# Performance work log

Hardware: AMD Instinct MI355X
Metric: run time of the kernel (lower is better)

Reference implementation:

```python
import jax, jax.numpy as jnp
import numpy as np

B, C_IN, T = 32, 192, 8192
H, N_PH, OUT = 192, 1024, 4
EPS = 1e-5


def setup_inputs() -> dict:
    key = jax.random.key(0)
    ks = jax.random.split(key, 12)
    s = 0.02
    return {
        "x": jax.random.normal(ks[0], (B, C_IN, T), jnp.float32),
        "x_mask": jnp.ones((B, 1, N_PH), jnp.float32),
        "w": jax.random.randint(ks[1], (B, 1, N_PH), 0, 8, jnp.int32),
        "pre_w": jax.random.normal(ks[2], (H, C_IN), jnp.float32) * s,
        "pre_b": jnp.zeros((H,), jnp.float32),
        "conv0_w": jax.random.normal(ks[3], (H, H, 3), jnp.float32) * s,
        "conv0_b": jnp.zeros((H,), jnp.float32),
        "ln0_g": jnp.ones((H,), jnp.float32),
        "ln0_b": jnp.zeros((H,), jnp.float32),
        "conv1_w": jax.random.normal(ks[4], (H, H, 3), jnp.float32) * s,
        "conv1_b": jnp.zeros((H,), jnp.float32),
        "ln1_g": jnp.ones((H,), jnp.float32),
        "ln1_b": jnp.zeros((H,), jnp.float32),
        "lin_w": jax.random.normal(ks[5], (OUT, H), jnp.float32) * s,
        "lin_b": jnp.zeros((OUT,), jnp.float32),
    }


def _segment_mean(x, w2):
    # x: [B, C, T] frames; w2: [B, n_ph] int durations.
    # Faithful to the torch double loop: phoneme j pools frames
    # [cumsum(w)[j-1] : cumsum(w)[j]); w==0 -> zeros.
    ends = jnp.cumsum(w2, axis=1)                      # [B, n_ph]
    t = jnp.arange(x.shape[2], dtype=ends.dtype)       # [T]
    ph_id = jax.vmap(lambda e: jnp.searchsorted(e, t, side="right"))(ends)  # [B, T]
    # segment sums over frames; extra segment n_ph catches out-of-range frames
    sums = jax.vmap(lambda xt, ids: jax.ops.segment_sum(xt, ids, num_segments=N_PH + 1))(
        x.transpose(0, 2, 1), ph_id
    )                                                  # [B, n_ph+1, C]
    sums = sums[:, :N_PH].transpose(0, 2, 1)           # [B, C, n_ph]
    denom = jnp.maximum(w2, 1).astype(x.dtype)[:, None, :]
    return jnp.where(w2[:, None, :] > 0, sums / denom, 0.0)


def _conv3(x, k, b):
    y = jax.lax.conv_general_dilated(x, k, (1,), [(1, 1)],
                                     dimension_numbers=("NCH", "OIH", "NCH"))
    return y + b[None, :, None]


def _ln(x, g, b):
    # channel-dim LayerNorm for [B, C, T] (VITS modules.LayerNorm)
    m = jnp.mean(x, axis=1, keepdims=True)
    v = jnp.mean(jnp.square(x - m), axis=1, keepdims=True)
    return (x - m) * jax.lax.rsqrt(v + EPS) * g[None, :, None] + b[None, :, None]


def reference(x, x_mask, w, pre_w, pre_b, conv0_w, conv0_b, ln0_g, ln0_b,
              conv1_w, conv1_b, ln1_g, ln1_b, lin_w, lin_b):
    w2 = w.reshape(w.shape[0], -1).astype(jnp.int32)
    spec = _segment_mean(x, w2)                                 # [B, C_in, n_ph]
    h = jnp.einsum("bct,hc->bht", spec, pre_w) + pre_b[None, :, None]
    # block 0: conv -> relu -> LN (dropout is identity at eval), mask before each layer
    h = _conv3(h * x_mask, conv0_w, conv0_b)
    h = jax.nn.relu(h * x_mask)
    h = _ln(h * x_mask, ln0_g, ln0_b)
    h = h * x_mask  # dropout(p=0.1) at eval = identity; mask still applied
    # block 1
    h = _conv3(h * x_mask, conv1_w, conv1_b)
    h = jax.nn.relu(h * x_mask)
    h = _ln(h * x_mask, ln1_g, ln1_b)
    h = h * x_mask
    p = jnp.einsum("bht,oh->bot", h, lin_w) + lin_b[None, :, None]
    return p * x_mask
```

## Files before the change

kernel.cpp:

```cpp
#include <hip/hip_runtime.h>
#include <hip/hip_bf16.h>

#define B 32
#define C_IN 192
#define T 8192
#define H 192
#define N_PH 1024
#define OUT 4
#define ROW_MAX 7168
#define PROWS (N_PH + 2)
#define ROWP (2 * H)

typedef __attribute__((ext_vector_type(8))) short short8;
typedef __attribute__((ext_vector_type(4))) float f32x4;
typedef unsigned short ushort_t;

__device__ inline ushort_t f2bf(float f) {
    unsigned u = __builtin_bit_cast(unsigned, f);
    unsigned r = u + 0x7fffu + ((u >> 16) & 1u);
    return (ushort_t)(r >> 16);
}
__device__ inline float bf2f(ushort_t h) {
    unsigned u = ((unsigned)h) << 16;
    return __builtin_bit_cast(float, u);
}
__device__ inline void split_bf(float x, ushort_t& hi, ushort_t& lo) {
    hi = f2bf(x);
    lo = f2bf(x - bf2f(hi));
}

__global__ __launch_bounds__(256) void segmean_kernel(const float* __restrict__ x,
                                                      const int* __restrict__ wdur,
                                                      float* __restrict__ spec) {
    int bc = blockIdx.x;
    int b = bc / C_IN;
    int c = bc % C_IN;
    __shared__ int e_s[N_PH];
    __shared__ int part[256];
    __shared__ float row[ROW_MAX];
    int tid = threadIdx.x;
    int4 w4 = ((const int4*)(wdur + b * N_PH))[tid];
    int c0 = w4.x, c1 = c0 + w4.y, c2 = c1 + w4.z, c3 = c2 + w4.w;
    part[tid] = c3;
    __syncthreads();
    for (int off = 1; off < 256; off <<= 1) {
        int v = (tid >= off) ? part[tid - off] : 0;
        __syncthreads();
        part[tid] += v;
        __syncthreads();
    }
    int pre = tid ? part[tid - 1] : 0;
    e_s[4 * tid + 0] = pre + c0;
    e_s[4 * tid + 1] = pre + c1;
    e_s[4 * tid + 2] = pre + c2;
    e_s[4 * tid + 3] = pre + c3;
    __syncthreads();
    int emax = e_s[N_PH - 1];
    const float4* xr4 = (const float4*)(x + ((size_t)b * C_IN + c) * T);
    float4* row4 = (float4*)row;
    int nv = (emax + 3) >> 2;
    for (int t = tid; t < nv; t += 256) row4[t] = xr4[t];
    __syncthreads();
    float* sp = spec + ((size_t)b * C_IN + c) * N_PH;
    for (int j = tid; j < N_PH; j += 256) {
        int s0 = j ? e_s[j - 1] : 0;
        int e0 = e_s[j];
        float sum = 0.f;
        for (int t = s0; t < e0; ++t) sum += row[t];
        sp[j] = (e0 > s0) ? sum / (float)(e0 - s0) : 0.f;
    }
}

__global__ __launch_bounds__(256) void transpose_spec_kernel(const float* __restrict__ spec,
                                                             ushort_t* __restrict__ specT) {
    int jt = blockIdx.x * 32;
    int ct = (blockIdx.y % (C_IN / 32)) * 32;
    int b  = blockIdx.y / (C_IN / 32);
    __shared__ float tile[32][33];
    int tx = threadIdx.x & 31;
    int ty = threadIdx.x >> 5;
    const float* sb = spec + ((size_t)b * C_IN + ct) * N_PH + jt;
    for (int r = ty; r < 32; r += 8) tile[r][tx] = sb[(size_t)r * N_PH + tx];
    __syncthreads();
    ushort_t* ob = specT + ((size_t)b * N_PH + jt) * ROWP + ct;
    for (int r = ty; r < 32; r += 8) {
        ushort_t hi, lo;
        split_bf(tile[tx][r], hi, lo);
        ob[(size_t)r * ROWP + tx] = hi;
        ob[(size_t)r * ROWP + H + tx] = lo;
    }
}

__device__ inline void wfrag_one(const float* __restrict__ w, ushort_t* __restrict__ wtf,
                                 int taps, int idx, int ntot) {
    int j  = idx & 7;
    int l  = (idx >> 3) & 63;
    int slot = idx >> 9;
    int nt = slot % 12;
    int ss = (slot / 12) % 6;
    int kt = slot / 72;
    int o  = nt * 16 + (l & 15);
    int i  = ss * 32 + ((l >> 4) << 3) + j;
    float v = (taps == 1) ? w[o * C_IN + i] : w[(o * H + i) * 3 + kt];
    ushort_t hi, lo;
    split_bf(v, hi, lo);
    wtf[idx] = hi;
    wtf[idx + ntot] = lo;
}
__global__ void wfrag_all_kernel(const float* __restrict__ pw, const float* __restrict__ w0,
                                 const float* __restrict__ w1,
                                 ushort_t* __restrict__ wpre, ushort_t* __restrict__ w0t,
                                 ushort_t* __restrict__ w1t) {
    int idx = blockIdx.x * 256 + threadIdx.x;
    const int n1 = 36864, n3 = 110592;
    if (idx < n1) { wfrag_one(pw, wpre, 1, idx, n1); return; }
    idx -= n1;
    if (idx < n3) { wfrag_one(w0, w0t, 3, idx, n3); return; }
    idx -= n3;
    if (idx < n3) wfrag_one(w1, w1t, 3, idx, n3);
}

#define LOADOPS(IT, AH0, AL0, AH1, AL1, BH, BL) do {                              \
    int kt_ = (IT) / 6, s_ = (IT) - kt_ * 6;                                      \
    const ushort_t* arow_ = inb + (long)(trow + kt_ - pad) * ROWP + s_ * 32 + kg; \
    AH0 = *(const short8*)(arow_);                                                \
    AL0 = *(const short8*)(arow_ + H);                                            \
    AH1 = *(const short8*)(arow_ + 16 * ROWP);                                    \
    AL1 = *(const short8*)(arow_ + 16 * ROWP + H);                                \
    const ushort_t* wb_ = wt + ((size_t)((kt_ * 6 + s_) * 12 + nhalf * 6) << 9)   \
                        + (lane << 3);                                            \
    _Pragma("unroll") for (int n_ = 0; n_ < 6; ++n_) {                            \
        BH[n_] = *(const short8*)(wb_ + (n_ << 9));                               \
        BL[n_] = *(const short8*)(wb_ + (n_ << 9) + ntotw); }                     \
} while (0)

#define DOMFMA(AH0, AL0, AH1, AL1, BH, BL) do {                                             \
    _Pragma("unroll") for (int n_ = 0; n_ < 6; ++n_) {                                      \
        acc[0][n_] = __builtin_amdgcn_mfma_f32_16x16x32_bf16(AH0, BH[n_], acc[0][n_], 0,0,0); \
        acc[0][n_] = __builtin_amdgcn_mfma_f32_16x16x32_bf16(AL0, BH[n_], acc[0][n_], 0,0,0); \
        acc[0][n_] = __builtin_amdgcn_mfma_f32_16x16x32_bf16(AH0, BL[n_], acc[0][n_], 0,0,0); \
        acc[1][n_] = __builtin_amdgcn_mfma_f32_16x16x32_bf16(AH1, BH[n_], acc[1][n_], 0,0,0); \
        acc[1][n_] = __builtin_amdgcn_mfma_f32_16x16x32_bf16(AL1, BH[n_], acc[1][n_], 0,0,0); \
        acc[1][n_] = __builtin_amdgcn_mfma_f32_16x16x32_bf16(AH1, BL[n_], acc[1][n_], 0,0,0); } \
} while (0)

__global__ __launch_bounds__(256) void gemm_fused_kernel(
    const ushort_t* __restrict__ in, int in_rows,
    const ushort_t* __restrict__ wt,
    const float* __restrict__ bias,
    const float* __restrict__ mask,
    const float* __restrict__ g, const float* __restrict__ beta,
    ushort_t* __restrict__ out,
    const float* __restrict__ lw, const float* __restrict__ lb,
    float* __restrict__ fout,
    int taps, int do_ln, int nmask, int fin)
{
    int b  = blockIdx.y;
    int t0 = blockIdx.x * 64;
    int tid = threadIdx.x;
    int lane = tid & 63;
    int wv = tid >> 6;
    int mhalf = wv & 1;
    int nhalf = wv >> 1;

    __shared__ float ep[64][193];
    __shared__ float g_s[H], b_s[H], m_s[64], mstat[64], rstat[64];
    if (tid < H) { g_s[tid] = do_ln ? g[tid] : 1.f; b_s[tid] = do_ln ? beta[tid] : 0.f; }
    if (tid < 64) m_s[tid] = mask[b * N_PH + t0 + tid];

    short8 z8 = {0, 0, 0, 0, 0, 0, 0, 0};
    if (!fin) {
        if (t0 == 0 && tid < ROWP / 8)
            *(short8*)(out + (size_t)b * PROWS * ROWP + tid * 8) = z8;
        if (t0 == N_PH - 64 && tid < ROWP / 8)
            *(short8*)(out + ((size_t)b * PROWS + N_PH + 1) * ROWP + tid * 8) = z8;
    }

    int m  = lane & 15;
    int kg = (lane >> 4) << 3;
    int ntotw = taps * 36864;
    int pad = taps >> 1;

    const ushort_t* inb = in + (size_t)b * in_rows * ROWP;
    int trow = t0 + mhalf * 32 + m;

    f32x4 acc[2][6];
#pragma unroll
    for (int ntl = 0; ntl < 6; ++ntl) {
        float bb = bias[(nhalf * 6 + ntl) * 16 + m];
        acc[0][ntl] = (f32x4){bb, bb, bb, bb};
        acc[1][ntl] = (f32x4){bb, bb, bb, bb};
    }

    short8 pah0, pal0, pah1, pal1, pbh[6], pbl[6];
    short8 qah0, qal0, qah1, qal1, qbh[6], qbl[6];
    int iters = taps * 6;
    LOADOPS(0, pah0, pal0, pah1, pal1, pbh, pbl);
#pragma unroll 1
    for (int it = 0; it < iters; it += 2) {
        LOADOPS(it + 1, qah0, qal0, qah1, qal1, qbh, qbl);
        DOMFMA(pah0, pal0, pah1, pal1, pbh, pbl);
        if (it + 2 < iters) LOADOPS(it + 2, pah0, pal0, pah1, pal1, pbh, pbl);
        DOMFMA(qah0, qal0, qah1, qal1, qbh, qbl);
    }

    __syncthreads();

    int rbase = (lane >> 4) << 2;
#pragma unroll
    for (int mh = 0; mh < 2; ++mh) {
#pragma unroll
        for (int ntl = 0; ntl < 6; ++ntl) {
            int o = (nhalf * 6 + ntl) * 16 + m;
#pragma unroll
            for (int r = 0; r < 4; ++r) {
                int t_loc = mhalf * 32 + mh * 16 + rbase + r;
                float mm = m_s[t_loc];
                float v = acc[mh][ntl][r];
                if (do_ln) {
                    v = fmaxf(v * mm, 0.f) * mm;
                } else {
                    for (int q = 0; q < nmask; ++q) v *= mm;
                }
                ep[t_loc][o] = v;
            }
        }
    }
    __syncthreads();

    if (do_ln && tid < 64) {
        float s = 0.f, ss = 0.f;
        for (int c = 0; c < H; ++c) {
            float v = ep[tid][c];
            s += v;
            ss += v * v;
        }
        float mean = s * (1.f / (float)H);
        mstat[tid] = mean;
        rstat[tid] = rsqrtf(ss * (1.f / (float)H) - mean * mean + 1e-5f);
    }
    __syncthreads();

    int row = tid >> 2;
    int q = tid & 3;
    if (fin) {
        float mean = mstat[row], rstd = rstat[row], mk = m_s[row];
        float a0 = 0.f, a1 = 0.f, a2 = 0.f, a3 = 0.f;
#pragma unroll 1
        for (int c = q * 48; c < q * 48 + 48; ++c) {
            float y = ((ep[row][c] - mean) * rstd * g_s[c] + b_s[c]) * mk;
            a0 += lw[0 * H + c] * y;
            a1 += lw[1 * H + c] * y;
            a2 += lw[2 * H + c] * y;
            a3 += lw[3 * H + c] * y;
        }
        a0 += __shfl_xor(a0, 1); a0 += __shfl_xor(a0, 2);
        a1 += __shfl_xor(a1, 1); a1 += __shfl_xor(a1, 2);
        a2 += __shfl_xor(a2, 1); a2 += __shfl_xor(a2, 2);
        a3 += __shfl_xor(a3, 1); a3 += __shfl_xor(a3, 2);
        if (q == 0) {
            int t = t0 + row;
            float* ob = fout + (size_t)b * OUT * N_PH + t;
            ob[0 * N_PH] = (a0 + lb[0]) * mk;
            ob[1 * N_PH] = (a1 + lb[1]) * mk;
            ob[2 * N_PH] = (a2 + lb[2]) * mk;
            ob[3 * N_PH] = (a3 + lb[3]) * mk;
        }
        return;
    }

    float mean = 0.f, rstd = 1.f, mfac = 1.f;
    if (do_ln) {
        mean = mstat[row];
        rstd = rstat[row];
        float mk = m_s[row];
        mfac = (nmask == 2) ? mk * mk : mk;
    }
    ushort_t* orow = out + ((size_t)b * PROWS + t0 + row + 1) * ROWP + q * 48;
#pragma unroll
    for (int i0 = 0; i0 < 48; i0 += 8) {
        ushort_t th[8], tl[8];
#pragma unroll
        for (int k2 = 0; k2 < 8; ++k2) {
            int c = q * 48 + i0 + k2;
            float v = ep[row][c];
            float y = do_ln ? ((v - mean) * rstd * g_s[c] + b_s[c]) * mfac : v;
            split_bf(y, th[k2], tl[k2]);
        }
        *(short8*)(orow + i0) = *(short8*)th;
        *(short8*)(orow + H + i0) = *(short8*)tl;
    }
}

extern "C" void kernel_launch(void* const* d_in, const int* in_sizes, int n_in,
                              void* d_out, int out_size, void* d_ws, size_t ws_size,
                              hipStream_t stream) {
    const float* x      = (const float*)d_in[0];
    const float* x_mask = (const float*)d_in[1];
    const int*   w      = (const int*)d_in[2];
    const float* pre_w  = (const float*)d_in[3];
    const float* pre_b  = (const float*)d_in[4];
    const float* conv0_w = (const float*)d_in[5];
    const float* conv0_b = (const float*)d_in[6];
    const float* ln0_g   = (const float*)d_in[7];
    const float* ln0_b   = (const float*)d_in[8];
    const float* conv1_w = (const float*)d_in[9];
    const float* conv1_b = (const float*)d_in[10];
    const float* ln1_g   = (const float*)d_in[11];
    const float* ln1_b   = (const float*)d_in[12];
    const float* lin_w   = (const float*)d_in[13];
    const float* lin_b   = (const float*)d_in[14];
    float* out = (float*)d_out;

    char* ws = (char*)d_ws;
    size_t off = 0;
    float* spec = (float*)(ws + off);       off += (size_t)B * C_IN * N_PH * sizeof(float);
    ushort_t* bufA = (ushort_t*)(ws + off); off += (size_t)B * PROWS * ROWP * sizeof(ushort_t);
    ushort_t* bufB = (ushort_t*)(ws + off); off += (size_t)B * PROWS * ROWP * sizeof(ushort_t);
    ushort_t* wpre = (ushort_t*)(ws + off); off += (size_t)2 * 36864 * sizeof(ushort_t);
    ushort_t* w0t  = (ushort_t*)(ws + off); off += (size_t)2 * 110592 * sizeof(ushort_t);
    ushort_t* w1t  = (ushort_t*)(ws + off); off += (size_t)2 * 110592 * sizeof(ushort_t);
    ushort_t* specT = bufB;

    wfrag_all_kernel<<<(36864 + 2 * 110592 + 255) / 256, 256, 0, stream>>>(
        pre_w, conv0_w, conv1_w, wpre, w0t, w1t);

    segmean_kernel<<<B * C_IN, 256, 0, stream>>>(x, w, spec);
    dim3 gt(N_PH / 32, (C_IN / 32) * B);
    transpose_spec_kernel<<<gt, 256, 0, stream>>>(spec, specT);

    dim3 gg(N_PH / 64, B);
    gemm_fused_kernel<<<gg, 256, 0, stream>>>(specT, N_PH, wpre, pre_b, x_mask,
                                              ln0_g, ln0_b, bufA,
                                              nullptr, nullptr, nullptr, 1, 0, 1, 0);
    gemm_fused_kernel<<<gg, 256, 0, stream>>>(bufA + ROWP, PROWS, w0t, conv0_b, x_mask,
                                              ln0_g, ln0_b, bufB,
                                              nullptr, nullptr, nullptr, 3, 1, 2, 0);
    gemm_fused_kernel<<<gg, 256, 0, stream>>>(bufB + ROWP, PROWS, w1t, conv1_b, x_mask,
                                              ln1_g, ln1_b, bufA,
                                              lin_w, lin_b, out, 3, 1, 1, 1);
}
```

Baseline: 399.8 us.

## Fuse all stages into one persistent cooperative kernel with grid syncs

Replaces the six separate launches (weight fragment prep, segment mean, transpose, three GEMM stages) with a single cooperative persistent kernel whose blocks loop over work tiles and separate stages with grid.sync. Cumulative durations are computed once per batch into a workspace buffer instead of per (b,c) block. This targets launch overhead and inter-kernel gaps. The cost is fewer resident blocks (capped at 512) doing the GEMM stages, grid-wide barrier cost, and a shared-memory union sized for the largest stage, which may limit occupancy. The old multi-kernel path is kept as a fallback if the cooperative launch fails.

New measurement: 829.1 us. +107.4%, slower.

```diff
diff --git a/kernel.cpp b/kernel.cpp
--- a/kernel.cpp
+++ b/kernel.cpp
@@ -1,5 +1,8 @@
 #include <hip/hip_runtime.h>
 #include <hip/hip_bf16.h>
+#include <hip/hip_cooperative_groups.h>
+
+namespace cg = cooperative_groups;
 
 #define B 32
 #define C_IN 192
@@ -10,6 +13,7 @@
 #define ROW_MAX 7168
 #define PROWS (N_PH + 2)
 #define ROWP (2 * H)
+#define NCU 256
 
 typedef __attribute__((ext_vector_type(8))) short short8;
 typedef __attribute__((ext_vector_type(4))) float f32x4;
@@ -29,67 +33,11 @@
     lo = f2bf(x - bf2f(hi));
 }
 
-__global__ __launch_bounds__(256) void segmean_kernel(const float* __restrict__ x,
-                                                      const int* __restrict__ wdur,
-                                                      float* __restrict__ spec) {
-    int bc = blockIdx.x;
-    int b = bc / C_IN;
-    int c = bc % C_IN;
-    __shared__ int e_s[N_PH];
-    __shared__ int part[256];
-    __shared__ float row[ROW_MAX];
-    int tid = threadIdx.x;
-    int4 w4 = ((const int4*)(wdur + b * N_PH))[tid];
-    int c0 = w4.x, c1 = c0 + w4.y, c2 = c1 + w4.z, c3 = c2 + w4.w;
-    part[tid] = c3;
-    __syncthreads();
-    for (int off = 1; off < 256; off <<= 1) {
-        int v = (tid >= off) ? part[tid - off] : 0;
-        __syncthreads();
-        part[tid] += v;
-        __syncthreads();
-    }
-    int pre = tid ? part[tid - 1] : 0;
-    e_s[4 * tid + 0] = pre + c0;
-    e_s[4 * tid + 1] = pre + c1;
-    e_s[4 * tid + 2] = pre + c2;
-    e_s[4 * tid + 3] = pre + c3;
-    __syncthreads();
-    int emax = e_s[N_PH - 1];
-    const float4* xr4 = (const float4*)(x + ((size_t)b * C_IN + c) * T);
-    float4* row4 = (float4*)row;
-    int nv = (emax + 3) >> 2;
-    for (int t = tid; t < nv; t += 256) row4[t] = xr4[t];
-    __syncthreads();
-    float* sp = spec + ((size_t)b * C_IN + c) * N_PH;
-    for (int j = tid; j < N_PH; j += 256) {
-        int s0 = j ? e_s[j - 1] : 0;
-        int e0 = e_s[j];
-        float sum = 0.f;
-        for (int t = s0; t < e0; ++t) sum += row[t];
-        sp[j] = (e0 > s0) ? sum / (float)(e0 - s0) : 0.f;
-    }
-}
-
-__global__ __launch_bounds__(256) void transpose_spec_kernel(const float* __restrict__ spec,
-                                                             ushort_t* __restrict__ specT) {
-    int jt = blockIdx.x * 32;
-    int ct = (blockIdx.y % (C_IN / 32)) * 32;
-    int b  = blockIdx.y / (C_IN / 32);
-    __shared__ float tile[32][33];
-    int tx = threadIdx.x & 31;
-    int ty = threadIdx.x >> 5;
-    const float* sb = spec + ((size_t)b * C_IN + ct) * N_PH + jt;
-    for (int r = ty; r < 32; r += 8) tile[r][tx] = sb[(size_t)r * N_PH + tx];
-    __syncthreads();
-    ushort_t* ob = specT + ((size_t)b * N_PH + jt) * ROWP + ct;
-    for (int r = ty; r < 32; r += 8) {
-        ushort_t hi, lo;
-        split_bf(tile[tx][r], hi, lo);
-        ob[(size_t)r * ROWP + tx] = hi;
-        ob[(size_t)r * ROWP + H + tx] = lo;
-    }
-}
+struct S1 { int e_s[N_PH]; int part[256]; float row[ROW_MAX]; };
+struct S2 { float tile[32][33]; };
+struct S3 { float ep[64][193]; float g_s[H]; float b_s[H];
+            float m_s[64]; float mstat[64]; float rstat[64]; };
+union __align__(16) SharedU { S1 s1; S2 s2; S3 s3; };
 
 __device__ inline void wfrag_one(const float* __restrict__ w, ushort_t* __restrict__ wtf,
                                  int taps, int idx, int ntot) {
@@ -107,18 +55,6 @@
     wtf[idx] = hi;
     wtf[idx + ntot] = lo;
 }
-__global__ void wfrag_all_kernel(const float* __restrict__ pw, const float* __restrict__ w0,
-                                 const float* __restrict__ w1,
-                                 ushort_t* __restrict__ wpre, ushort_t* __restrict__ w0t,
-                                 ushort_t* __restrict__ w1t) {
-    int idx = blockIdx.x * 256 + threadIdx.x;
-    const int n1 = 36864, n3 = 110592;
-    if (idx < n1) { wfrag_one(pw, wpre, 1, idx, n1); return; }
-    idx -= n1;
-    if (idx < n3) { wfrag_one(w0, w0t, 3, idx, n3); return; }
-    idx -= n3;
-    if (idx < n3) wfrag_one(w1, w1t, 3, idx, n3);
-}
 
 #define LOADOPS(IT, AH0, AL0, AH1, AL1, BH, BL) do {                              \
     int kt_ = (IT) / 6, s_ = (IT) - kt_ * 6;                                      \
@@ -144,7 +80,7 @@
         acc[1][n_] = __builtin_amdgcn_mfma_f32_16x16x32_bf16(AH1, BL[n_], acc[1][n_], 0,0,0); } \
 } while (0)
 
-__global__ __launch_bounds__(256) void gemm_fused_kernel(
+__device__ void gemm_core(SharedU& sh, int tix,
     const ushort_t* __restrict__ in, int in_rows,
     const ushort_t* __restrict__ wt,
     const float* __restrict__ bias,
@@ -155,16 +91,23 @@
     float* __restrict__ fout,
     int taps, int do_ln, int nmask, int fin)
 {
-    int b  = blockIdx.y;
-    int t0 = blockIdx.x * 64;
+    int b  = tix >> 4;
+    int t0 = (tix & 15) * 64;
     int tid = threadIdx.x;
     int lane = tid & 63;
     int wv = tid >> 6;
     int mhalf = wv & 1;
     int nhalf = wv >> 1;
 
-    __shared__ float ep[64][193];
-    __shared__ float g_s[H], b_s[H], m_s[64], mstat[64], rstat[64];
+    float (&ep)[64][193] = sh.s3.ep;
+    float* g_s  = sh.s3.g_s;
+    float* b_s  = sh.s3.b_s;
+    float* m_s  = sh.s3.m_s;
+    float* mstat = sh.s3.mstat;
+    float* rstat = sh.s3.rstat;
+
+    __syncthreads();
+
     if (tid < H) { g_s[tid] = do_ln ? g[tid] : 1.f; b_s[tid] = do_ln ? beta[tid] : 0.f; }
     if (tid < 64) m_s[tid] = mask[b * N_PH + t0 + tid];
 
@@ -290,6 +233,210 @@
         *(short8*)(orow + i0) = *(short8*)th;
         *(short8*)(orow + H + i0) = *(short8*)tl;
     }
+}
+
+__global__ __launch_bounds__(256) void mega_kernel(
+    const float* __restrict__ x, const float* __restrict__ x_mask,
+    const int* __restrict__ wdur,
+    const float* __restrict__ pre_w, const float* __restrict__ pre_b,
+    const float* __restrict__ conv0_w, const float* __restrict__ conv0_b,
+    const float* __restrict__ ln0_g, const float* __restrict__ ln0_b,
+    const float* __restrict__ conv1_w, const float* __restrict__ conv1_b,
+    const float* __restrict__ ln1_g, const float* __restrict__ ln1_b,
+    const float* __restrict__ lin_w, const float* __restrict__ lin_b,
+    float* __restrict__ out,
+    float* __restrict__ spec, ushort_t* __restrict__ bufA, ushort_t* __restrict__ bufB,
+    ushort_t* __restrict__ wpre, ushort_t* __restrict__ w0t, ushort_t* __restrict__ w1t,
+    int* __restrict__ ends)
+{
+    cg::grid_group grid = cg::this_grid();
+    int blk = blockIdx.x;
+    int nblk = gridDim.x;
+    int tid = threadIdx.x;
+    __shared__ SharedU sh;
+    ushort_t* specT = bufB;
+
+    {
+        const int n1 = 36864, n3 = 110592;
+        for (int idx = blk * 256 + tid; idx < n1 + 2 * n3; idx += nblk * 256) {
+            int i2 = idx;
+            if (i2 < n1)              wfrag_one(pre_w, wpre, 1, i2, n1);
+            else if ((i2 -= n1) < n3) wfrag_one(conv0_w, w0t, 3, i2, n3);
+            else                      wfrag_one(conv1_w, w1t, 3, i2 - n3, n3);
+        }
+        if (blk < B) {
+            int b = blk;
+            int* part = sh.s1.part;
+            int4 w4 = ((const int4*)(wdur + b * N_PH))[tid];
+            int c0 = w4.x, c1 = c0 + w4.y, c2 = c1 + w4.z, c3 = c2 + w4.w;
+            part[tid] = c3;
+            __syncthreads();
+            for (int off = 1; off < 256; off <<= 1) {
+                int v = (tid >= off) ? part[tid - off] : 0;
+                __syncthreads();
+                part[tid] += v;
+                __syncthreads();
+            }
+            int pre = tid ? part[tid - 1] : 0;
+            int4 e4;
+            e4.x = pre + c0; e4.y = pre + c1; e4.z = pre + c2; e4.w = pre + c3;
+            ((int4*)(ends + b * N_PH))[tid] = e4;
+        }
+    }
+    __threadfence();
+    grid.sync();
+
+    for (int bc = blk; bc < B * C_IN; bc += nblk) {
+        int b = bc / C_IN;
+        int c = bc - b * C_IN;
+        ((int4*)sh.s1.e_s)[tid] = ((const int4*)(ends + b * N_PH))[tid];
+        __syncthreads();
+        int emax = sh.s1.e_s[N_PH - 1];
+        const float4* xr4 = (const float4*)(x + ((size_t)b * C_IN + c) * T);
+        float4* row4 = (float4*)sh.s1.row;
+        int nv = (emax + 3) >> 2;
+        for (int t2 = tid; t2 < nv; t2 += 256) row4[t2] = xr4[t2];
+        __syncthreads();
+        float* sp = spec + ((size_t)b * C_IN + c) * N_PH;
+        for (int j = tid; j < N_PH; j += 256) {
+            int s0 = j ? sh.s1.e_s[j - 1] : 0;
+            int e0 = sh.s1.e_s[j];
+            float sum = 0.f;
+            for (int t2 = s0; t2 < e0; ++t2) sum += sh.s1.row[t2];
+            sp[j] = (e0 > s0) ? sum / (float)(e0 - s0) : 0.f;
+        }
+        __syncthreads();
+    }
+    __threadfence();
+    grid.sync();
+
+    for (int tix2 = blk; tix2 < (N_PH / 32) * (C_IN / 32) * B; tix2 += nblk) {
+        int jt = (tix2 & 31) * 32;
+        int rem = tix2 >> 5;
+        int ct = (rem % (C_IN / 32)) * 32;
+        int b  = rem / (C_IN / 32);
+        int tx = tid & 31;
+        int ty = tid >> 5;
+        const float* sb = spec + ((size_t)b * C_IN + ct) * N_PH + jt;
+        for (int r = ty; r < 32; r += 8) sh.s2.tile[r][tx] = sb[(size_t)r * N_PH + tx];
+        __syncthreads();
+        ushort_t* ob = specT + ((size_t)b * N_PH + jt) * ROWP + ct;
+        for (int r = ty; r < 32; r += 8) {
+            ushort_t hi, lo;
+            split_bf(sh.s2.tile[tx][r], hi, lo);
+            ob[(size_t)r * ROWP + tx] = hi;
+            ob[(size_t)r * ROWP + H + tx] = lo;
+        }
+        __syncthreads();
+    }
+    __threadfence();
+    grid.sync();
+
+    for (int tix = blk; tix < 16 * B; tix += nblk)
+        gemm_core(sh, tix, specT, N_PH, wpre, pre_b, x_mask, ln0_g, ln0_b, bufA,
+                  nullptr, nullptr, nullptr, 1, 0, 1, 0);
+    __threadfence();
+    grid.sync();
+
+    for (int tix = blk; tix < 16 * B; tix += nblk)
+        gemm_core(sh, tix, bufA + ROWP, PROWS, w0t, conv0_b, x_mask, ln0_g, ln0_b, bufB,
+                  nullptr, nullptr, nullptr, 3, 1, 2, 0);
+    __threadfence();
+    grid.sync();
+
+    for (int tix = blk; tix < 16 * B; tix += nblk)
+        gemm_core(sh, tix, bufB + ROWP, PROWS, w1t, conv1_b, x_mask, ln1_g, ln1_b, bufA,
+                  lin_w, lin_b, out, 3, 1, 1, 1);
+}
+
+__global__ __launch_bounds__(256) void segmean_kernel(const float* __restrict__ x,
+                                                      const int* __restrict__ wdur,
+                                                      float* __restrict__ spec) {
+    int bc = blockIdx.x;
+    int b = bc / C_IN;
+    int c = bc % C_IN;
+    __shared__ SharedU sh;
+    int tid = threadIdx.x;
+    int4 w4 = ((const int4*)(wdur + b * N_PH))[tid];
+    int c0 = w4.x, c1 = c0 + w4.y, c2 = c1 + w4.z, c3 = c2 + w4.w;
+    sh.s1.part[tid] = c3;
+    __syncthreads();
+    for (int off = 1; off < 256; off <<= 1) {
+        int v = (tid >= off) ? sh.s1.part[tid - off] : 0;
+        __syncthreads();
+        sh.s1.part[tid] += v;
+        __syncthreads();
+    }
+    int pre = tid ? sh.s1.part[tid - 1] : 0;
+    sh.s1.e_s[4 * tid + 0] = pre + c0;
+    sh.s1.e_s[4 * tid + 1] = pre + c1;
+    sh.s1.e_s[4 * tid + 2] = pre + c2;
+    sh.s1.e_s[4 * tid + 3] = pre + c3;
+    __syncthreads();
+    int emax = sh.s1.e_s[N_PH - 1];
+    const float4* xr4 = (const float4*)(x + ((size_t)b * C_IN + c) * T);
+    float4* row4 = (float4*)sh.s1.row;
+    int nv = (emax + 3) >> 2;
+    for (int t2 = tid; t2 < nv; t2 += 256) row4[t2] = xr4[t2];
+    __syncthreads();
+    float* sp = spec + ((size_t)b * C_IN + c) * N_PH;
+    for (int j = tid; j < N_PH; j += 256) {
+        int s0 = j ? sh.s1.e_s[j - 1] : 0;
+        int e0 = sh.s1.e_s[j];
+        float sum = 0.f;
+        for (int t2 = s0; t2 < e0; ++t2) sum += sh.s1.row[t2];
+        sp[j] = (e0 > s0) ? sum / (float)(e0 - s0) : 0.f;
+    }
+}
+
+__global__ __launch_bounds__(256) void transpose_spec_kernel(const float* __restrict__ spec,
+                                                             ushort_t* __restrict__ specT) {
+    int jt = blockIdx.x * 32;
+    int ct = (blockIdx.y % (C_IN / 32)) * 32;
+    int b  = blockIdx.y / (C_IN / 32);
+    __shared__ SharedU sh;
+    int tx = threadIdx.x & 31;
+    int ty = threadIdx.x >> 5;
+    const float* sb = spec + ((size_t)b * C_IN + ct) * N_PH + jt;
+    for (int r = ty; r < 32; r += 8) sh.s2.tile[r][tx] = sb[(size_t)r * N_PH + tx];
+    __syncthreads();
+    ushort_t* ob = specT + ((size_t)b * N_PH + jt) * ROWP + ct;
+    for (int r = ty; r < 32; r += 8) {
+        ushort_t hi, lo;
+        split_bf(sh.s2.tile[tx][r], hi, lo);
+        ob[(size_t)r * ROWP + tx] = hi;
+        ob[(size_t)r * ROWP + H + tx] = lo;
+    }
+}
+
+__global__ void wfrag_all_kernel(const float* __restrict__ pw, const float* __restrict__ w0,
+                                 const float* __restrict__ w1,
+                                 ushort_t* __restrict__ wpre, ushort_t* __restrict__ w0t,
+                                 ushort_t* __restrict__ w1t) {
+    int idx = blockIdx.x * 256 + threadIdx.x;
+    const int n1 = 36864, n3 = 110592;
+    if (idx < n1) { wfrag_one(pw, wpre, 1, idx, n1); return; }
+    idx -= n1;
+    if (idx < n3) { wfrag_one(w0, w0t, 3, idx, n3); return; }
+    idx -= n3;
+    if (idx < n3) wfrag_one(w1, w1t, 3, idx, n3);
+}
+
+__global__ __launch_bounds__(256) void gemm_fused_kernel(
+    const ushort_t* __restrict__ in, int in_rows,
+    const ushort_t* __restrict__ wt,
+    const float* __restrict__ bias,
+    const float* __restrict__ mask,
+    const float* __restrict__ g, const float* __restrict__ beta,
+    ushort_t* __restrict__ out,
+    const float* __restrict__ lw, const float* __restrict__ lb,
+    float* __restrict__ fout,
+    int taps, int do_ln, int nmask, int fin)
+{
+    __shared__ SharedU sh;
+    int tix = blockIdx.y * (N_PH / 64) + blockIdx.x;
+    gemm_core(sh, tix, in, in_rows, wt, bias, mask, g, beta, out, lw, lb, fout,
+              taps, do_ln, nmask, fin);
 }
 
 extern "C" void kernel_launch(void* const* d_in, const int* in_sizes, int n_in,
@@ -320,15 +467,34 @@
     ushort_t* wpre = (ushort_t*)(ws + off); off += (size_t)2 * 36864 * sizeof(ushort_t);
     ushort_t* w0t  = (ushort_t*)(ws + off); off += (size_t)2 * 110592 * sizeof(ushort_t);
     ushort_t* w1t  = (ushort_t*)(ws + off); off += (size_t)2 * 110592 * sizeof(ushort_t);
+    int* ends      = (int*)(ws + off);      off += (size_t)B * N_PH * sizeof(int);
     ushort_t* specT = bufB;
+
+    int maxb = 0;
+    hipError_t qe = hipOccupancyMaxActiveBlocksPerMultiprocessor(&maxb, mega_kernel, 256, 0);
+    if (qe != hipSuccess || maxb < 1) maxb = 1;
+    int nblk = maxb * NCU;
+    if (nblk > 512) nblk = 512;
+
+    void* kargs[] = {
+        (void*)&x, (void*)&x_mask, (void*)&w,
+        (void*)&pre_w, (void*)&pre_b,
+        (void*)&conv0_w, (void*)&conv0_b, (void*)&ln0_g, (void*)&ln0_b,
+        (void*)&conv1_w, (void*)&conv1_b, (void*)&ln1_g, (void*)&ln1_b,
+        (void*)&lin_w, (void*)&lin_b, (void*)&out,
+        (void*)&spec, (void*)&bufA, (void*)&bufB,
+        (void*)&wpre, (void*)&w0t, (void*)&w1t, (void*)&ends
+    };
+    hipError_t le = hipLaunchCooperativeKernel((const void*)mega_kernel, dim3(nblk),
+                                               dim3(256), kargs, 0, stream);
+    if (le == hipSuccess) return;
+    (void)hipGetLastError();
 
     wfrag_all_kernel<<<(36864 + 2 * 110592 + 255) / 256, 256, 0, stream>>>(
         pre_w, conv0_w, conv1_w, wpre, w0t, w1t);
-
     segmean_kernel<<<B * C_IN, 256, 0, stream>>>(x, w, spec);
     dim3 gt(N_PH / 32, (C_IN / 32) * B);
     transpose_spec_kernel<<<gt, 256, 0, stream>>>(spec, specT);
-
     dim3 gg(N_PH / 64, B);
     gemm_fused_kernel<<<gg, 256, 0, stream>>>(specT, N_PH, wpre, pre_b, x_mask,
                                               ln0_g, ln0_b, bufA,
```

## Fuse segment-mean with transpose and bf16 split, hoist duration cumsum into prep

Applied to the files above, without the earlier changes.

Drops the per-channel segmean kernel and the separate transpose kernel. A prep kernel now builds the weight fragments and computes the duration prefix sums once per batch. A new kernel then pools frames straight from global memory for 32 phonemes by 192 channels, transposes in LDS and writes the hi/lo bf16 specT rows. This removes the float spec intermediate round trip, one launch and the cumsum that was redundantly recomputed for every channel. In exchange, x loads are per-thread variable-length gathers with divergent loop lengths rather than coalesced float4 row loads.

Result: no change. 401.8 us (+0.5%).

```diff
diff --git a/kernel.cpp b/kernel.cpp
--- a/kernel.cpp
+++ b/kernel.cpp
@@ -7,7 +7,6 @@
 #define H 192
 #define N_PH 1024
 #define OUT 4
-#define ROW_MAX 7168
 #define PROWS (N_PH + 2)
 #define ROWP (2 * H)
 
@@ -27,68 +26,6 @@
 __device__ inline void split_bf(float x, ushort_t& hi, ushort_t& lo) {
     hi = f2bf(x);
     lo = f2bf(x - bf2f(hi));
-}
-
-__global__ __launch_bounds__(256) void segmean_kernel(const float* __restrict__ x,
-                                                      const int* __restrict__ wdur,
-                                                      float* __restrict__ spec) {
-    int bc = blockIdx.x;
-    int b = bc / C_IN;
-    int c = bc % C_IN;
-    __shared__ int e_s[N_PH];
-    __shared__ int part[256];
-    __shared__ float row[ROW_MAX];
-    int tid = threadIdx.x;
-    int4 w4 = ((const int4*)(wdur + b * N_PH))[tid];
-    int c0 = w4.x, c1 = c0 + w4.y, c2 = c1 + w4.z, c3 = c2 + w4.w;
-    part[tid] = c3;
-    __syncthreads();
-    for (int off = 1; off < 256; off <<= 1) {
-        int v = (tid >= off) ? part[tid - off] : 0;
-        __syncthreads();
-        part[tid] += v;
-        __syncthreads();
-    }
-    int pre = tid ? part[tid - 1] : 0;
-    e_s[4 * tid + 0] = pre + c0;
-    e_s[4 * tid + 1] = pre + c1;
-    e_s[4 * tid + 2] = pre + c2;
-    e_s[4 * tid + 3] = pre + c3;
-    __syncthreads();
-    int emax = e_s[N_PH - 1];
-    const float4* xr4 = (const float4*)(x + ((size_t)b * C_IN + c) * T);
-    float4* row4 = (float4*)row;
-    int nv = (emax + 3) >> 2;
-    for (int t = tid; t < nv; t += 256) row4[t] = xr4[t];
-    __syncthreads();
-    float* sp = spec + ((size_t)b * C_IN + c) * N_PH;
-    for (int j = tid; j < N_PH; j += 256) {
-        int s0 = j ? e_s[j - 1] : 0;
-        int e0 = e_s[j];
-        float sum = 0.f;
-        for (int t = s0; t < e0; ++t) sum += row[t];
-        sp[j] = (e0 > s0) ? sum / (float)(e0 - s0) : 0.f;
-    }
-}
-
-__global__ __launch_bounds__(256) void transpose_spec_kernel(const float* __restrict__ spec,
-                                                             ushort_t* __restrict__ specT) {
-    int jt = blockIdx.x * 32;
-    int ct = (blockIdx.y % (C_IN / 32)) * 32;
-    int b  = blockIdx.y / (C_IN / 32);
-    __shared__ float tile[32][33];
-    int tx = threadIdx.x & 31;
-    int ty = threadIdx.x >> 5;
-    const float* sb = spec + ((size_t)b * C_IN + ct) * N_PH + jt;
-    for (int r = ty; r < 32; r += 8) tile[r][tx] = sb[(size_t)r * N_PH + tx];
-    __syncthreads();
-    ushort_t* ob = specT + ((size_t)b * N_PH + jt) * ROWP + ct;
-    for (int r = ty; r < 32; r += 8) {
-        ushort_t hi, lo;
-        split_bf(tile[tx][r], hi, lo);
-        ob[(size_t)r * ROWP + tx] = hi;
-        ob[(size_t)r * ROWP + H + tx] = lo;
-    }
 }
 
 __device__ inline void wfrag_one(const float* __restrict__ w, ushort_t* __restrict__ wtf,
@@ -107,17 +44,87 @@
     wtf[idx] = hi;
     wtf[idx + ntot] = lo;
 }
-__global__ void wfrag_all_kernel(const float* __restrict__ pw, const float* __restrict__ w0,
-                                 const float* __restrict__ w1,
-                                 ushort_t* __restrict__ wpre, ushort_t* __restrict__ w0t,
-                                 ushort_t* __restrict__ w1t) {
-    int idx = blockIdx.x * 256 + threadIdx.x;
+
+#define NWF 1008
+__global__ __launch_bounds__(256) void prep_kernel(
+    const float* __restrict__ pw, const float* __restrict__ w0,
+    const float* __restrict__ w1, const int* __restrict__ wdur,
+    ushort_t* __restrict__ wpre, ushort_t* __restrict__ w0t,
+    ushort_t* __restrict__ w1t, int* __restrict__ ends)
+{
+    int blk = blockIdx.x;
+    int tid = threadIdx.x;
     const int n1 = 36864, n3 = 110592;
-    if (idx < n1) { wfrag_one(pw, wpre, 1, idx, n1); return; }
-    idx -= n1;
-    if (idx < n3) { wfrag_one(w0, w0t, 3, idx, n3); return; }
-    idx -= n3;
-    if (idx < n3) wfrag_one(w1, w1t, 3, idx, n3);
+    if (blk < NWF) {
+        int idx = blk * 256 + tid;
+        if (idx < n1) { wfrag_one(pw, wpre, 1, idx, n1); return; }
+        idx -= n1;
+        if (idx < n3) { wfrag_one(w0, w0t, 3, idx, n3); return; }
+        idx -= n3;
+        if (idx < n3) wfrag_one(w1, w1t, 3, idx, n3);
+        return;
+    }
+    int b = blk - NWF;
+    __shared__ int part[256];
+    int4 w4 = ((const int4*)(wdur + b * N_PH))[tid];
+    int c0 = w4.x, c1 = c0 + w4.y, c2 = c1 + w4.z, c3 = c2 + w4.w;
+    part[tid] = c3;
+    __syncthreads();
+    for (int off = 1; off < 256; off <<= 1) {
+        int v = (tid >= off) ? part[tid - off] : 0;
+        __syncthreads();
+        part[tid] += v;
+        __syncthreads();
+    }
+    int pre = tid ? part[tid - 1] : 0;
+    int4 e4;
+    e4.x = pre + c0; e4.y = pre + c1; e4.z = pre + c2; e4.w = pre + c3;
+    ((int4*)(ends + b * N_PH))[tid] = e4;
+}
+
+__global__ __launch_bounds__(256) void segmean_direct_kernel(
+    const float* __restrict__ x, const int* __restrict__ ends,
+    ushort_t* __restrict__ specT)
+{
+    int b  = blockIdx.x >> 5;
+    int jt = (blockIdx.x & 31) * 32;
+    int tid = threadIdx.x;
+    int j_loc = tid & 31;
+    int cg0 = tid >> 5;
+    int j = jt + j_loc;
+
+    __shared__ float sm[32][193];
+
+    const int* eb = ends + b * N_PH;
+    int e0 = eb[j];
+    int s0 = j ? eb[j - 1] : 0;
+    int len = e0 - s0;
+    float inv = (len > 0) ? 1.f / (float)len : 0.f;
+
+    const float* xb = x + (size_t)b * C_IN * T;
+#pragma unroll 1
+    for (int c = cg0; c < C_IN; c += 8) {
+        const float* xr = xb + (size_t)c * T;
+        float sum = 0.f;
+        for (int t = s0; t < e0; ++t) sum += xr[t];
+        sm[j_loc][c] = sum * inv;
+    }
+    __syncthreads();
+
+    int r = tid >> 3;
+    int g = tid & 7;
+    ushort_t* ob = specT + ((size_t)b * N_PH + jt + r) * ROWP;
+#pragma unroll
+    for (int i0 = 0; i0 < 24; i0 += 8) {
+        ushort_t th[8], tl[8];
+#pragma unroll
+        for (int k2 = 0; k2 < 8; ++k2) {
+            int c = g * 24 + i0 + k2;
+            split_bf(sm[r][c], th[k2], tl[k2]);
+        }
+        *(short8*)(ob + g * 24 + i0) = *(short8*)th;
+        *(short8*)(ob + H + g * 24 + i0) = *(short8*)tl;
+    }
 }
 
 #define LOADOPS(IT, AH0, AL0, AH1, AL1, BH, BL) do {                              \
@@ -314,20 +321,18 @@
 
     char* ws = (char*)d_ws;
     size_t off = 0;
-    float* spec = (float*)(ws + off);       off += (size_t)B * C_IN * N_PH * sizeof(float);
     ushort_t* bufA = (ushort_t*)(ws + off); off += (size_t)B * PROWS * ROWP * sizeof(ushort_t);
     ushort_t* bufB = (ushort_t*)(ws + off); off += (size_t)B * PROWS * ROWP * sizeof(ushort_t);
     ushort_t* wpre = (ushort_t*)(ws + off); off += (size_t)2 * 36864 * sizeof(ushort_t);
     ushort_t* w0t  = (ushort_t*)(ws + off); off += (size_t)2 * 110592 * sizeof(ushort_t);
     ushort_t* w1t  = (ushort_t*)(ws + off); off += (size_t)2 * 110592 * sizeof(ushort_t);
+    int* ends      = (int*)(ws + off);      off += (size_t)B * N_PH * sizeof(int);
     ushort_t* specT = bufB;
 
-    wfrag_all_kernel<<<(36864 + 2 * 110592 + 255) / 256, 256, 0, stream>>>(
-        pre_w, conv0_w, conv1_w, wpre, w0t, w1t);
-
-    segmean_kernel<<<B * C_IN, 256, 0, stream>>>(x, w, spec);
-    dim3 gt(N_PH / 32, (C_IN / 32) * B);
-    transpose_spec_kernel<<<gt, 256, 0, stream>>>(spec, specT);
+    prep_kernel<<<NWF + B, 256, 0, stream>>>(pre_w, conv0_w, conv1_w, w,
+                                             wpre, w0t, w1t, ends);
+
+    segmean_direct_kernel<<<B * 32, 256, 0, stream>>>(x, ends, specT);
 
     dim3 gg(N_PH / 64, B);
     gemm_fused_kernel<<<gg, 256, 0, stream>>>(specT, N_PH, wpre, pre_b, x_mask,
```
